# Kernel tuning notes

Measured on AMD Instinct MI355X. Metric: run time of the kernel, lower is better.

Reference implementation:

```python
import jax, jax.numpy as jnp
import numpy as np

K = 1.0          # curvature of all manifolds
EPS = 1e-6
LN_EPS = 1e-5    # torch LayerNorm eps
POWER_K = 3.0

N_NODES, N_EDGES, IN_DIM, HID, HEADS = 50000, 250000, 128, 32, 4


def _time(s):
    # Lorentz time coordinate from space part
    return jnp.sqrt(jnp.sum(s * s, axis=-1, keepdims=True) + K)


def _hyp_point(s):
    return jnp.concatenate([_time(s), s], axis=-1)


def _layernorm(s, g, b):
    m = jnp.mean(s, axis=-1, keepdims=True)
    v = jnp.var(s, axis=-1, keepdims=True)
    return (s - m) / jnp.sqrt(v + LN_EPS) * g + b


def _fp(x, p=POWER_K):
    # ||x||_2 / ||x^p||_2 * x^p  (TransConv.fp)
    nx = jnp.sqrt(jnp.sum(x * x, axis=-1, keepdims=True))
    xp = x ** p
    nxp = jnp.sqrt(jnp.sum(xp * xp, axis=-1, keepdims=True))
    return nx / nxp * xp


def setup_inputs() -> dict:
    key = jax.random.key(0)
    ks = jax.random.split(key, 12)
    f32 = jnp.float32
    inp = {
        'h': jax.random.normal(ks[0], (N_NODES, IN_DIM), f32),
        'src': jax.random.randint(ks[1], (N_EDGES,), 0, N_NODES, jnp.int32),
        'dst': jax.random.randint(ks[2], (N_EDGES,), 0, N_NODES, jnp.int32),
        # fcs[0][0]: HypLinear(in_dim -> hidden), euclidean input (+1 time col)
        'W_fc': (jax.random.normal(ks[3], (IN_DIM + 1, HID), f32) / np.float32(np.sqrt(IN_DIM + 1))),
        'b_fc': jnp.zeros((HID,), f32),
        # bns[0]: HypLayerNorm(hidden)
        'ln1_g': jnp.ones((HID,), f32), 'ln1_b': jnp.zeros((HID,), f32),
        # Wq/Wk/Wv: per-head HypLinear(hidden -> hidden), input is (hidden+1)-dim point
        'Wq': jax.random.normal(ks[4], (HEADS, HID + 1, HID), f32) / np.float32(np.sqrt(HID + 1)),
        'bq': jnp.zeros((HEADS, HID), f32),
        'Wk': jax.random.normal(ks[5], (HEADS, HID + 1, HID), f32) / np.float32(np.sqrt(HID + 1)),
        'bk': jnp.zeros((HEADS, HID), f32),
        'Wv': jax.random.normal(ks[6], (HEADS, HID + 1, HID), f32) / np.float32(np.sqrt(HID + 1)),
        'bv': jnp.zeros((HEADS, HID), f32),
        # hidden_to_out[0]: HypLinear(hidden -> hidden)
        'W_ho': jax.random.normal(ks[7], (HID + 1, HID), f32) / np.float32(np.sqrt(HID + 1)),
        'b_ho': jnp.zeros((HID,), f32),
        # final HypLayerNorm (self.bn)
        'ln2_g': jnp.ones((HID,), f32), 'ln2_b': jnp.zeros((HID,), f32),
        'norm_scale': jnp.ones((), f32),
    }
    return inp


def reference(h, src, dst, W_fc, b_fc, ln1_g, ln1_b, Wq, bq, Wk, bk, Wv, bv,
              W_ho, b_ho, ln2_g, ln2_b, norm_scale):
    N = h.shape[0]
    # iter == 0: lift euclidean features, prepend ones for time column
    x1 = jnp.concatenate([jnp.ones_like(h[..., :1]), h], axis=-1)  # [N, IN+1]
    hyp = _hyp_point(x1 @ W_fc + b_fc)                             # [N, HID+1]
    residual = hyp
    # HypLayerNorm -> HypActivation(leaky_relu) -> HypDropout (eval: identity).
    # Intermediate time coords are recomputed/discarded; only the final point's
    # full (HID+1) coords feed the q/k/v HypLinears.
    s = jax.nn.leaky_relu(_layernorm(hyp[..., 1:], ln1_g, ln1_b))
    node = _hyp_point(s)                                           # [N, HID+1]
    # per-head HypLinear; edge_attention only uses the space part [:, :, 1:],
    # so the q/k/v time coords are never consumed and are omitted here.
    q = jnp.einsum('nt,htd->nhd', node, Wq) + bq                   # [N, H, HID]
    k = jnp.einsum('nt,htd->nhd', node, Wk) + bk
    v = jnp.einsum('nt,htd->nhd', node, Wv) + bv
    # gather to edges
    qe = q[dst]                                                    # [E, H, HID]
    ke = k[src]
    ve = v[src]
    inv_scale = 1.0 / jnp.abs(norm_scale)
    phi_q = _fp((jax.nn.leaky_relu(qe) + EPS) * inv_scale)
    phi_k = _fp((jax.nn.leaky_relu(ke) + EPS) * inv_scale)
    phi_v = (jax.nn.leaky_relu(ve) + EPS) * inv_scale
    # global (over all edges) kernelized linear attention moments
    ktv = jnp.einsum('ehm,ehd->hmd', phi_k, phi_v)                 # [H, HID, HID]
    numerator = jnp.einsum('ehm,hmd->ehd', phi_q, ktv)             # [E, H, HID]
    denominator = jnp.einsum('ehd,hd->eh', phi_q, jnp.sum(phi_k, axis=0))[..., None]
    attn = jnp.mean(numerator / (denominator + EPS), axis=1)       # [E, HID]
    t = jnp.sqrt(jnp.sum(attn * attn, axis=-1, keepdims=True) + K)
    edge_in = jnp.concatenate([t, attn], axis=-1)                  # [E, HID+1]
    edge_out = _hyp_point(edge_in @ W_ho + b_ho)                   # [E, HID+1]
    # fn.copy_e + fn.mean over incoming edges per destination node
    seg_sum = jax.ops.segment_sum(edge_out, dst, num_segments=N)
    cnt = jax.ops.segment_sum(jnp.ones((edge_out.shape[0], 1), edge_out.dtype), dst, num_segments=N)
    agg = jnp.where(cnt > 0, seg_sum / jnp.maximum(cnt, 1.0), 0.0)
    # Lorentz mid_point of (agg, residual)
    ave = 0.5 * (agg + residual)
    inner = -ave[..., :1] ** 2 + jnp.sum(ave[..., 1:] ** 2, axis=-1, keepdims=True)
    denom = jnp.sqrt(jnp.maximum(jnp.abs(inner), EPS))
    hnew = jnp.sqrt(K) * ave / denom
    # final HypLayerNorm + HypDropout(eval)
    out = _hyp_point(_layernorm(hnew[..., 1:], ln2_g, ln2_b))
    return out
```

## Files before the change

kernel.cpp:

```cpp
#include <hip/hip_runtime.h>

#define NN 50000
#define NE 250000
#define KTVC 4224
#define NBX 512

__device__ __forceinline__ float lrelu(float x) { return x > 0.f ? x : 0.01f * x; }

__global__ __launch_bounds__(256) void k_hist(const int* __restrict__ src,
                                              const int* __restrict__ dst,
                                              int* __restrict__ cnt_src,
                                              int* __restrict__ cnt_dst) {
    int e = blockIdx.x * 256 + threadIdx.x;
    if (e < NE) {
        atomicAdd(&cnt_src[src[e]], 1);
        atomicAdd(&cnt_dst[dst[e]], 1);
    }
}

__global__ __launch_bounds__(512) void k_fc(const float* __restrict__ h,
                                            const float* __restrict__ Wfc,
                                            const float* __restrict__ bfc,
                                            const float* __restrict__ g1,
                                            const float* __restrict__ b1,
                                            float* __restrict__ resid,
                                            float* __restrict__ node33T) {
    __shared__ float hch[128][33];
    __shared__ float stat_t[8][128];
    __shared__ float stat2_t[4][128];
    const int tid = threadIdx.x;
    const int q = __builtin_amdgcn_readfirstlane((threadIdx.x >> 7) & 3);
    const int nl = tid & 127;
    const int base = blockIdx.x * 128;
    const int n = base + nl;

    float acc[8];
#pragma unroll
    for (int jj = 0; jj < 8; ++jj) acc[jj] = Wfc[q * 8 + jj] + bfc[q * 8 + jj];

    for (int c = 0; c < 4; ++c) {
        __syncthreads();
#pragma unroll
        for (int r = 0; r < 8; ++r) {
            int idx = r * 512 + tid;
            int sn = idx >> 5, t = idx & 31;
            int gn = base + sn;
            hch[sn][t] = h[(size_t)((gn < NN) ? gn : 0) * 128 + c * 32 + t];
        }
        __syncthreads();
        for (int i = 0; i < 32; ++i) {
            float hv = hch[nl][i];
            const float* wr = Wfc + (size_t)(1 + c * 32 + i) * 32 + q * 8;
#pragma unroll
            for (int jj = 0; jj < 8; ++jj) acc[jj] = fmaf(hv, wr[jj], acc[jj]);
        }
    }
    float ps = 0.f, pq2 = 0.f;
#pragma unroll
    for (int jj = 0; jj < 8; ++jj) { ps += acc[jj]; pq2 += acc[jj] * acc[jj]; }
    stat_t[q * 2 + 0][nl] = ps;
    stat_t[q * 2 + 1][nl] = pq2;
    __syncthreads();
    float sm = stat_t[0][nl] + stat_t[2][nl] + stat_t[4][nl] + stat_t[6][nl];
    float sq = stat_t[1][nl] + stat_t[3][nl] + stat_t[5][nl] + stat_t[7][nl];
    float mean = sm * (1.f / 32.f);
    float var = fmaxf(sq * (1.f / 32.f) - mean * mean, 0.f);
    float rstd = rsqrtf(var + 1e-5f);
    float lr[8];
    float pl2 = 0.f;
#pragma unroll
    for (int jj = 0; jj < 8; ++jj) {
        int j = q * 8 + jj;
        float ln = (acc[jj] - mean) * rstd * g1[j] + b1[j];
        lr[jj] = lrelu(ln);
        pl2 += lr[jj] * lr[jj];
    }
    stat2_t[q][nl] = pl2;
    __syncthreads();
    float l2 = stat2_t[0][nl] + stat2_t[1][nl] + stat2_t[2][nl] + stat2_t[3][nl];
    if (n < NN) {
        float* rrow = resid + (size_t)n * 36;
#pragma unroll
        for (int jj = 0; jj < 8; ++jj) rrow[1 + q * 8 + jj] = acc[jj];
#pragma unroll
        for (int jj = 0; jj < 8; ++jj) node33T[(size_t)(1 + q * 8 + jj) * NN + n] = lr[jj];
        if (q == 0) {
            rrow[0] = sqrtf(sq + 1.f);
            node33T[n] = sqrtf(l2 + 1.f);
        }
    }
}

__global__ __launch_bounds__(128) void k_qkv(const float* __restrict__ node33T,
                                             const float* __restrict__ Wk, const float* __restrict__ bk,
                                             const float* __restrict__ Wv, const float* __restrict__ bv,
                                             const float* __restrict__ nscale,
                                             const int* __restrict__ cnt_src,
                                             float* __restrict__ partial) {
    __shared__ float nlds[64][33];
    __shared__ float pk[64][36];
    __shared__ float pv[64][36];
    const int tid = threadIdx.x;
    const int w_u = __builtin_amdgcn_readfirstlane(tid >> 6);
    const int h_u = __builtin_amdgcn_readfirstlane(blockIdx.y);
    const int lane = tid & 63;
    const float inv = 1.f / fabsf(nscale[0]);
    const float* W = ((w_u == 0) ? Wk : Wv) + (size_t)h_u * 33 * 32;
    const float* bb = ((w_u == 0) ? bk : bv) + h_u * 32;
    const int mm4 = lane >> 3, d4 = lane & 7;

    float facc[16];
#pragma unroll
    for (int t = 0; t < 16; ++t) facc[t] = 0.f;
    float ks[4] = {0.f, 0.f, 0.f, 0.f};

    const int ntiles = (NN + 63) / 64;
    for (int tile = blockIdx.x; tile < ntiles; tile += NBX) {
        const int base = tile * 64;
        const int n = base + lane;
        for (int idx = tid; idx < 2112; idx += 128) {
            int c = idx >> 6, sn = idx & 63;
            int gn = base + sn;
            nlds[sn][c] = node33T[(size_t)c * NN + ((gn < NN) ? gn : 0)];
        }
        __syncthreads();

        float acc[32];
#pragma unroll
        for (int j = 0; j < 32; ++j) acc[j] = bb[j];
        for (int i = 0; i < 33; ++i) {
            float hv = nlds[lane][i];
            const float* wr = W + (size_t)i * 32;
#pragma unroll
            for (int j = 0; j < 32; ++j) acc[j] = fmaf(hv, wr[j], acc[j]);
        }

        if (w_u == 0) {
            const float wc = (n < NN) ? (float)cnt_src[n] : 0.f;
            float s2 = 0.f, s6 = 0.f;
#pragma unroll
            for (int j = 0; j < 32; ++j) {
                float x = (lrelu(acc[j]) + 1e-6f) * inv;
                s2 += x * x;
                float x3 = x * x * x;
                s6 += x3 * x3;
                acc[j] = x3;
            }
            const float factor = sqrtf(s2) / sqrtf(s6) * wc;
#pragma unroll
            for (int j = 0; j < 32; ++j) pk[lane][j] = factor * acc[j];
        } else {
#pragma unroll
            for (int j = 0; j < 32; ++j) pv[lane][j] = (lrelu(acc[j]) + 1e-6f) * inv;
        }
        __syncthreads();

#pragma unroll 4
        for (int n0 = 0; n0 < 32; ++n0) {
            const int nn = w_u * 32 + n0;
            float4 pkv = *(const float4*)&pk[nn][mm4 * 4];
            float4 pvv = *(const float4*)&pv[nn][d4 * 4];
            float pkv_a[4] = {pkv.x, pkv.y, pkv.z, pkv.w};
            float pvv_a[4] = {pvv.x, pvv.y, pvv.z, pvv.w};
#pragma unroll
            for (int i = 0; i < 4; ++i)
#pragma unroll
                for (int jj = 0; jj < 4; ++jj)
                    facc[i * 4 + jj] = fmaf(pkv_a[i], pvv_a[jj], facc[i * 4 + jj]);
            if (d4 == 0) {
#pragma unroll
                for (int i = 0; i < 4; ++i) ks[i] += pkv_a[i];
            }
        }
        __syncthreads();
    }

    float* scr = &pk[0][0];
    float* scr2 = &pv[0][0];
    if (w_u == 0) {
#pragma unroll
        for (int t = 0; t < 16; ++t) scr[lane * 16 + t] = facc[t];
        if (d4 == 0) {
#pragma unroll
            for (int i = 0; i < 4; ++i) scr2[mm4 * 4 + i] = ks[i];
        }
    }
    __syncthreads();
    if (w_u == 1) {
        float* pb = partial + (size_t)blockIdx.x * KTVC + h_u * 1056;
#pragma unroll
        for (int i = 0; i < 4; ++i)
#pragma unroll
            for (int jj = 0; jj < 4; ++jj)
                pb[(mm4 * 4 + i) * 32 + d4 * 4 + jj] =
                    facc[i * 4 + jj] + scr[lane * 16 + i * 4 + jj];
        if (d4 == 0) {
#pragma unroll
            for (int i = 0; i < 4; ++i)
                pb[1024 + mm4 * 4 + i] = ks[i] + scr2[mm4 * 4 + i];
        }
    }
}

__global__ __launch_bounds__(256) void k_red(const float* __restrict__ partial,
                                             float* __restrict__ ktvf) {
    __shared__ float red[8][33];
    const int tid = threadIdx.x;
    const int col = tid & 31, g = tid >> 5;
    const int c = blockIdx.x * 32 + col;
    float s = 0.f;
    for (int r = g * 64; r < (g + 1) * 64; ++r)
        s += partial[(size_t)r * KTVC + c];
    red[g][col] = s;
    __syncthreads();
    if (tid < 32) {
        float t0 = (red[0][tid] + red[1][tid]) + (red[2][tid] + red[3][tid]);
        float t1 = (red[4][tid] + red[5][tid]) + (red[6][tid] + red[7][tid]);
        ktvf[blockIdx.x * 32 + tid] = t0 + t1;
    }
}

__global__ __launch_bounds__(256) void k_final(const float* __restrict__ node33T,
                                               const float* __restrict__ Wq, const float* __restrict__ bq,
                                               const float* __restrict__ nscale,
                                               const float* __restrict__ ktvf,
                                               const float* __restrict__ Who,
                                               const float* __restrict__ bho,
                                               const float* __restrict__ g2,
                                               const float* __restrict__ b2,
                                               const int* __restrict__ cnt_dst,
                                               const float* __restrict__ resid,
                                               float* __restrict__ out) {
    __shared__ float nlds[64][37];
    __shared__ float att[4][64][33];
    __shared__ float who_lds[33 * 32];
    __shared__ float g2l[32], b2l[32], bhol[32];
    const int tid = threadIdx.x;
    const int h_u = __builtin_amdgcn_readfirstlane(tid >> 6);
    const int lane = tid & 63;
    const int base = blockIdx.x * 64;
    const float inv = 1.f / fabsf(nscale[0]);

#pragma unroll
    for (int r = 0; r < 9; ++r) {
        int idx = r * 256 + tid;
        if (idx < 2112) {
            int c = idx >> 6, sn = idx & 63;
            int gn = base + sn;
            nlds[sn][c] = node33T[(size_t)c * NN + ((gn < NN) ? gn : 0)];
        }
    }
    for (int f = tid; f < 33 * 32; f += 256) who_lds[f] = Who[f];
    if (tid < 32) { g2l[tid] = g2[tid]; b2l[tid] = b2[tid]; bhol[tid] = bho[tid]; }
    __syncthreads();

    {
        float acc[32];
#pragma unroll
        for (int j = 0; j < 32; ++j) acc[j] = bq[h_u * 32 + j];
        const float* W = Wq + (size_t)h_u * 33 * 32;
        for (int i = 0; i < 33; ++i) {
            float hv = nlds[lane][i];
            const float* wr = W + (size_t)i * 32;
#pragma unroll
            for (int j = 0; j < 32; ++j) acc[j] = fmaf(hv, wr[j], acc[j]);
        }
        float s2 = 0.f, s6 = 0.f;
#pragma unroll
        for (int j = 0; j < 32; ++j) {
            float x = (lrelu(acc[j]) + 1e-6f) * inv;
            s2 += x * x;
            float x3 = x * x * x;
            s6 += x3 * x3;
            acc[j] = x3;
        }
        const float factor = sqrtf(s2) / sqrtf(s6);
        const float* ksum = ktvf + h_u * 1056 + 1024;
        float den = 0.f;
#pragma unroll
        for (int j = 0; j < 32; ++j) { acc[j] *= factor; den += acc[j] * ksum[j]; }
        const float rd = 0.25f / (den + 1e-6f);
        float num[32];
#pragma unroll
        for (int d = 0; d < 32; ++d) num[d] = 0.f;
        const float* kt = ktvf + h_u * 1056;
#pragma unroll 2
        for (int t = 0; t < 32; ++t) {
            const float f = acc[t];
            const float* kr = kt + t * 32;
#pragma unroll
            for (int d = 0; d < 32; ++d) num[d] = fmaf(f, kr[d], num[d]);
        }
#pragma unroll
        for (int d = 0; d < 32; ++d) att[h_u][lane][d] = num[d] * rd;
    }
    __syncthreads();

    const int nl2 = tid >> 2, jq = tid & 3;
    const int n2 = base + nl2;
    const int nc = (n2 < NN) ? n2 : NN - 1;
    float attn[32];
#pragma unroll
    for (int d = 0; d < 32; ++d)
        attn[d] = ((att[0][nl2][d] + att[1][nl2][d]) + (att[2][nl2][d] + att[3][nl2][d]));
    float a2 = 0.f;
#pragma unroll
    for (int d = 0; d < 32; ++d) a2 += attn[d] * attn[d];
    const float tc = sqrtf(a2 + 1.f);
    float eo[8];
#pragma unroll
    for (int jj = 0; jj < 8; ++jj) {
        int j = jq * 8 + jj;
        eo[jj] = bhol[j] + tc * who_lds[j];
    }
#pragma unroll
    for (int d = 0; d < 32; ++d) {
        const float f = attn[d];
        const float* wr = &who_lds[(1 + d) * 32 + jq * 8];
#pragma unroll
        for (int jj = 0; jj < 8; ++jj) eo[jj] = fmaf(f, wr[jj], eo[jj]);
    }
    float e2 = 0.f;
#pragma unroll
    for (int jj = 0; jj < 8; ++jj) e2 += eo[jj] * eo[jj];
    e2 += __shfl_xor(e2, 1);
    e2 += __shfl_xor(e2, 2);
    const float te = sqrtf(e2 + 1.f);
    const float sc = (cnt_dst[nc] > 0) ? 1.f : 0.f;
    const float* rr = resid + (size_t)nc * 36;
    const float av0 = 0.5f * (sc * te + rr[0]);
    float avs[8];
    float pinner = 0.f;
#pragma unroll
    for (int jj = 0; jj < 8; ++jj) {
        avs[jj] = 0.5f * (sc * eo[jj] + rr[1 + jq * 8 + jj]);
        pinner += avs[jj] * avs[jj];
    }
    pinner += __shfl_xor(pinner, 1);
    pinner += __shfl_xor(pinner, 2);
    const float inner = pinner - av0 * av0;
    const float rdn = 1.f / sqrtf(fmaxf(fabsf(inner), 1e-6f));
    float pm = 0.f;
#pragma unroll
    for (int jj = 0; jj < 8; ++jj) { avs[jj] *= rdn; pm += avs[jj]; }
    pm += __shfl_xor(pm, 1);
    pm += __shfl_xor(pm, 2);
    const float mean = pm * (1.f / 32.f);
    float pv2 = 0.f;
#pragma unroll
    for (int jj = 0; jj < 8; ++jj) { float dd = avs[jj] - mean; pv2 += dd * dd; }
    pv2 += __shfl_xor(pv2, 1);
    pv2 += __shfl_xor(pv2, 2);
    const float rstd = rsqrtf(pv2 * (1.f / 32.f) + 1e-5f);
    float ln[8];
    float pl2 = 0.f;
#pragma unroll
    for (int jj = 0; jj < 8; ++jj) {
        int j = jq * 8 + jj;
        ln[jj] = (avs[jj] - mean) * rstd * g2l[j] + b2l[j];
        pl2 += ln[jj] * ln[jj];
    }
    pl2 += __shfl_xor(pl2, 1);
    pl2 += __shfl_xor(pl2, 2);
    if (n2 < NN) {
        float* orow = out + (size_t)n2 * 33;
#pragma unroll
        for (int jj = 0; jj < 8; ++jj) orow[1 + jq * 8 + jj] = ln[jj];
        if (jq == 0) orow[0] = sqrtf(pl2 + 1.f);
    }
}

extern "C" void kernel_launch(void* const* d_in, const int* in_sizes, int n_in,
                              void* d_out, int out_size, void* d_ws, size_t ws_size,
                              hipStream_t stream) {
    const float* h   = (const float*)d_in[0];
    const int* src   = (const int*)d_in[1];
    const int* dst   = (const int*)d_in[2];
    const float* Wfc = (const float*)d_in[3];
    const float* bfc = (const float*)d_in[4];
    const float* g1  = (const float*)d_in[5];
    const float* b1  = (const float*)d_in[6];
    const float* Wq  = (const float*)d_in[7];
    const float* bq  = (const float*)d_in[8];
    const float* Wk  = (const float*)d_in[9];
    const float* bk  = (const float*)d_in[10];
    const float* Wv  = (const float*)d_in[11];
    const float* bv  = (const float*)d_in[12];
    const float* Who = (const float*)d_in[13];
    const float* bho = (const float*)d_in[14];
    const float* g2  = (const float*)d_in[15];
    const float* b2  = (const float*)d_in[16];
    const float* nsc = (const float*)d_in[17];
    float* out = (float*)d_out;
    char* ws = (char*)d_ws;

    int* cnt_src   = (int*)(ws + 0);
    int* cnt_dst   = (int*)(ws + 200000);
    float* resid   = (float*)(ws + 400000);
    float* node33T = (float*)(ws + 7600000);
    float* part    = (float*)(ws + 14200000);
    float* ktvf    = (float*)(ws + 22852608);

    hipMemsetAsync(ws, 0, 400000, stream);
    hipLaunchKernelGGL(k_hist, dim3((NE + 255) / 256), dim3(256), 0, stream,
                       src, dst, cnt_src, cnt_dst);
    hipLaunchKernelGGL(k_fc, dim3((NN + 127) / 128), dim3(512), 0, stream,
                       h, Wfc, bfc, g1, b1, resid, node33T);
    hipLaunchKernelGGL(k_qkv, dim3(NBX, 4), dim3(128), 0, stream,
                       node33T, Wk, bk, Wv, bv, nsc, cnt_src, part);
    hipLaunchKernelGGL(k_red, dim3(KTVC / 32), dim3(256), 0, stream,
                       part, ktvf);
    hipLaunchKernelGGL(k_final, dim3((NN + 63) / 64), dim3(256), 0, stream,
                       node33T, Wq, bq, nsc, ktvf, Who, bho, g2, b2, cnt_dst, resid, out);
}
```

Baseline: 126.9 us.

## Use one k_qkv block per tile and load node features straight into registers

k_qkv drops its grid-stride loop over tiles and launches one block per 64-node tile. The k_red partial reduction is widened to cover the larger number of partial rows, and the ktvf buffer is moved to make room. Both k_qkv and k_final now read the 33 node features per lane directly from the transposed global array into registers instead of staging them through LDS, which removes one LDS buffer and a barrier. hipMemsetAsync is replaced by a small zeroing kernel. The partial buffer grows and the reduction reads more rows; the per-lane column loads and larger register arrays may raise register pressure.

```diff
diff --git a/kernel.cpp b/kernel.cpp
--- a/kernel.cpp
+++ b/kernel.cpp
@@ -3,9 +3,14 @@
 #define NN 50000
 #define NE 250000
 #define KTVC 4224
-#define NBX 512
+#define NTILES 782
 
 __device__ __forceinline__ float lrelu(float x) { return x > 0.f ? x : 0.01f * x; }
+
+__global__ __launch_bounds__(256) void k_zero(int* __restrict__ p) {
+    int i = blockIdx.x * 256 + threadIdx.x;
+    if (i < 100000) p[i] = 0;
+}
 
 __global__ __launch_bounds__(256) void k_hist(const int* __restrict__ src,
                                               const int* __restrict__ dst,
@@ -97,9 +102,8 @@
                                              const float* __restrict__ nscale,
                                              const int* __restrict__ cnt_src,
                                              float* __restrict__ partial) {
-    __shared__ float nlds[64][33];
-    __shared__ float pk[64][36];
-    __shared__ float pv[64][36];
+    __shared__ float pk[64][33];
+    __shared__ float pv[64][33];
     const int tid = threadIdx.x;
     const int w_u = __builtin_amdgcn_readfirstlane(tid >> 6);
     const int h_u = __builtin_amdgcn_readfirstlane(blockIdx.y);
@@ -109,71 +113,66 @@
     const float* bb = ((w_u == 0) ? bk : bv) + h_u * 32;
     const int mm4 = lane >> 3, d4 = lane & 7;
 
+    const int base = blockIdx.x * 64;
+    const int n = base + lane;
+    const int nc = (n < NN) ? n : 0;
+
+    float nvec[33];
+#pragma unroll
+    for (int c = 0; c < 33; ++c) nvec[c] = node33T[(size_t)c * NN + nc];
+
+    float acc[32];
+#pragma unroll
+    for (int j = 0; j < 32; ++j) acc[j] = bb[j];
+    for (int i = 0; i < 33; ++i) {
+        const float* wr = W + (size_t)i * 32;
+#pragma unroll
+        for (int j = 0; j < 32; ++j) acc[j] = fmaf(nvec[i], wr[j], acc[j]);
+    }
+
+    if (w_u == 0) {
+        const float wc = (n < NN) ? (float)cnt_src[n] : 0.f;
+        float s2 = 0.f, s6 = 0.f;
+#pragma unroll
+        for (int j = 0; j < 32; ++j) {
+            float x = (lrelu(acc[j]) + 1e-6f) * inv;
+            s2 += x * x;
+            float x3 = x * x * x;
+            s6 += x3 * x3;
+            acc[j] = x3;
+        }
+        const float factor = sqrtf(s2) / sqrtf(s6) * wc;
+#pragma unroll
+        for (int j = 0; j < 32; ++j) pk[lane][j] = factor * acc[j];
+    } else {
+#pragma unroll
+        for (int j = 0; j < 32; ++j) pv[lane][j] = (lrelu(acc[j]) + 1e-6f) * inv;
+    }
+    __syncthreads();
+
     float facc[16];
 #pragma unroll
     for (int t = 0; t < 16; ++t) facc[t] = 0.f;
     float ks[4] = {0.f, 0.f, 0.f, 0.f};
-
-    const int ntiles = (NN + 63) / 64;
-    for (int tile = blockIdx.x; tile < ntiles; tile += NBX) {
-        const int base = tile * 64;
-        const int n = base + lane;
-        for (int idx = tid; idx < 2112; idx += 128) {
-            int c = idx >> 6, sn = idx & 63;
-            int gn = base + sn;
-            nlds[sn][c] = node33T[(size_t)c * NN + ((gn < NN) ? gn : 0)];
-        }
-        __syncthreads();
-
-        float acc[32];
-#pragma unroll
-        for (int j = 0; j < 32; ++j) acc[j] = bb[j];
-        for (int i = 0; i < 33; ++i) {
-            float hv = nlds[lane][i];
-            const float* wr = W + (size_t)i * 32;
-#pragma unroll
-            for (int j = 0; j < 32; ++j) acc[j] = fmaf(hv, wr[j], acc[j]);
-        }
-
-        if (w_u == 0) {
-            const float wc = (n < NN) ? (float)cnt_src[n] : 0.f;
-            float s2 = 0.f, s6 = 0.f;
-#pragma unroll
-            for (int j = 0; j < 32; ++j) {
-                float x = (lrelu(acc[j]) + 1e-6f) * inv;
-                s2 += x * x;
-                float x3 = x * x * x;
-                s6 += x3 * x3;
-                acc[j] = x3;
-            }
-            const float factor = sqrtf(s2) / sqrtf(s6) * wc;
-#pragma unroll
-            for (int j = 0; j < 32; ++j) pk[lane][j] = factor * acc[j];
-        } else {
-#pragma unroll
-            for (int j = 0; j < 32; ++j) pv[lane][j] = (lrelu(acc[j]) + 1e-6f) * inv;
-        }
-        __syncthreads();
-
 #pragma unroll 4
-        for (int n0 = 0; n0 < 32; ++n0) {
-            const int nn = w_u * 32 + n0;
-            float4 pkv = *(const float4*)&pk[nn][mm4 * 4];
-            float4 pvv = *(const float4*)&pv[nn][d4 * 4];
-            float pkv_a[4] = {pkv.x, pkv.y, pkv.z, pkv.w};
-            float pvv_a[4] = {pvv.x, pvv.y, pvv.z, pvv.w};
-#pragma unroll
-            for (int i = 0; i < 4; ++i)
-#pragma unroll
-                for (int jj = 0; jj < 4; ++jj)
-                    facc[i * 4 + jj] = fmaf(pkv_a[i], pvv_a[jj], facc[i * 4 + jj]);
-            if (d4 == 0) {
-#pragma unroll
-                for (int i = 0; i < 4; ++i) ks[i] += pkv_a[i];
-            }
-        }
-        __syncthreads();
-    }
+    for (int n0 = 0; n0 < 32; ++n0) {
+        const int nn = w_u * 32 + n0;
+        float pkv_a[4], pvv_a[4];
+#pragma unroll
+        for (int i = 0; i < 4; ++i) pkv_a[i] = pk[nn][mm4 * 4 + i];
+#pragma unroll
+        for (int i = 0; i < 4; ++i) pvv_a[i] = pv[nn][d4 * 4 + i];
+#pragma unroll
+        for (int i = 0; i < 4; ++i)
+#pragma unroll
+            for (int jj = 0; jj < 4; ++jj)
+                facc[i * 4 + jj] = fmaf(pkv_a[i], pvv_a[jj], facc[i * 4 + jj]);
+        if (d4 == 0) {
+#pragma unroll
+            for (int i = 0; i < 4; ++i) ks[i] += pkv_a[i];
+        }
+    }
+    __syncthreads();
 
     float* scr = &pk[0][0];
     float* scr2 = &pv[0][0];
@@ -208,8 +207,9 @@
     const int tid = threadIdx.x;
     const int col = tid & 31, g = tid >> 5;
     const int c = blockIdx.x * 32 + col;
+    const int r0 = g * 98, r1 = min(r0 + 98, NTILES);
     float s = 0.f;
-    for (int r = g * 64; r < (g + 1) * 64; ++r)
+    for (int r = r0; r < r1; ++r)
         s += partial[(size_t)r * KTVC + c];
     red[g][col] = s;
     __syncthreads();
@@ -231,7 +231,6 @@
                                                const int* __restrict__ cnt_dst,
                                                const float* __restrict__ resid,
                                                float* __restrict__ out) {
-    __shared__ float nlds[64][37];
     __shared__ float att[4][64][33];
     __shared__ float who_lds[33 * 32];
     __shared__ float g2l[32], b2l[32], bhol[32];
@@ -240,30 +239,24 @@
     const int lane = tid & 63;
     const int base = blockIdx.x * 64;
     const float inv = 1.f / fabsf(nscale[0]);
-
-#pragma unroll
-    for (int r = 0; r < 9; ++r) {
-        int idx = r * 256 + tid;
-        if (idx < 2112) {
-            int c = idx >> 6, sn = idx & 63;
-            int gn = base + sn;
-            nlds[sn][c] = node33T[(size_t)c * NN + ((gn < NN) ? gn : 0)];
-        }
-    }
+    const int n = base + lane;
+    const int ncl = (n < NN) ? n : 0;
+
     for (int f = tid; f < 33 * 32; f += 256) who_lds[f] = Who[f];
     if (tid < 32) { g2l[tid] = g2[tid]; b2l[tid] = b2[tid]; bhol[tid] = bho[tid]; }
-    __syncthreads();
 
     {
+        float nvec[33];
+#pragma unroll
+        for (int c = 0; c < 33; ++c) nvec[c] = node33T[(size_t)c * NN + ncl];
         float acc[32];
 #pragma unroll
         for (int j = 0; j < 32; ++j) acc[j] = bq[h_u * 32 + j];
         const float* W = Wq + (size_t)h_u * 33 * 32;
         for (int i = 0; i < 33; ++i) {
-            float hv = nlds[lane][i];
             const float* wr = W + (size_t)i * 32;
 #pragma unroll
-            for (int j = 0; j < 32; ++j) acc[j] = fmaf(hv, wr[j], acc[j]);
+            for (int j = 0; j < 32; ++j) acc[j] = fmaf(nvec[i], wr[j], acc[j]);
         }
         float s2 = 0.f, s6 = 0.f;
 #pragma unroll
@@ -399,14 +392,14 @@
     float* resid   = (float*)(ws + 400000);
     float* node33T = (float*)(ws + 7600000);
     float* part    = (float*)(ws + 14200000);
-    float* ktvf    = (float*)(ws + 22852608);
-
-    hipMemsetAsync(ws, 0, 400000, stream);
+    float* ktvf    = (float*)(ws + 27412672);
+
+    hipLaunchKernelGGL(k_zero, dim3(391), dim3(256), 0, stream, (int*)ws);
     hipLaunchKernelGGL(k_hist, dim3((NE + 255) / 256), dim3(256), 0, stream,
                        src, dst, cnt_src, cnt_dst);
     hipLaunchKernelGGL(k_fc, dim3((NN + 127) / 128), dim3(512), 0, stream,
                        h, Wfc, bfc, g1, b1, resid, node33T);
-    hipLaunchKernelGGL(k_qkv, dim3(NBX, 4), dim3(128), 0, stream,
+    hipLaunchKernelGGL(k_qkv, dim3(NTILES, 4), dim3(128), 0, stream,
                        node33T, Wk, bk, Wv, bv, nsc, cnt_src, part);
     hipLaunchKernelGGL(k_red, dim3(KTVC / 32), dim3(256), 0, stream,
                        part, ktvf);
```

After: 131.9 us. 1.04x slower.
